# Performance work log

Hardware: AMD Instinct MI355X
Metric: run time of the kernel (lower is better)

Reference implementation:

```python
import jax, jax.numpy as jnp
import numpy as np

B, S, R, C_MSA, C_PAIR, H, D = 1, 128, 384, 256, 128, 8, 32
EPS = 1e-5


def setup_inputs() -> dict:
    key = jax.random.key(0)
    ks = jax.random.split(key, 8)
    w = 0.02
    return {
        "msa_repr": jax.random.normal(ks[0], (B, S, R, C_MSA), jnp.float32),
        "pair_repr": jax.random.normal(ks[1], (B, R, R, C_PAIR), jnp.float32),
        "ln_g": jnp.ones((R,), jnp.float32),
        "ln_b": jnp.zeros((R,), jnp.float32),
        "Wq": jax.random.normal(ks[2], (C_MSA, H * D), jnp.float32) * w,
        "Wk": jax.random.normal(ks[3], (C_MSA, H * D), jnp.float32) * w,
        "Wv": jax.random.normal(ks[4], (C_MSA, H * D), jnp.float32) * w,
        "Wb": jax.random.normal(ks[5], (C_PAIR, H), jnp.float32) * w,
        "bb": jnp.zeros((H,), jnp.float32),
        "Wg": jax.random.normal(ks[6], (C_MSA, H * D), jnp.float32) * w,
        "bg": jnp.zeros((H * D,), jnp.float32),
        "Wo": jax.random.normal(ks[7], (H * D, C_MSA), jnp.float32) * w,
        "bo": jnp.zeros((C_MSA,), jnp.float32),
    }


def reference(msa_repr, pair_repr, ln_g, ln_b, Wq, Wk, Wv, Wb, bb, Wg, bg, Wo, bo):
    b, s, r, c = msa_repr.shape
    scale = 1.0 / jnp.sqrt(jnp.float32(D))
    # LayerNorm over the residue axis r (module permutes b s r c -> b c s r and
    # normalizes the last dim = sequence_size), gamma/beta indexed by r.
    mu = jnp.mean(msa_repr, axis=2, keepdims=True)
    var = jnp.var(msa_repr, axis=2, keepdims=True)
    x = (msa_repr - mu) * jax.lax.rsqrt(var + EPS)
    x = x * ln_g[None, None, :, None] + ln_b[None, None, :, None]
    # flatten MSA rows into batch: (b*s, r, c)
    x = x.reshape(b * s, r, c)
    q = (x @ Wq).reshape(b * s, r, H, D).transpose(0, 2, 1, 3)  # (bs) h r d
    k = (x @ Wk).reshape(b * s, r, H, D).transpose(0, 2, 1, 3)
    v = (x @ Wv).reshape(b * s, r, H, D).transpose(0, 2, 1, 3)
    g = jax.nn.sigmoid(x @ Wg + bg).reshape(b * s, r, H, D).transpose(0, 2, 1, 3)
    # pair bias: b i j c -> b i j h -> b h i j, tiled over rows as in einops repeat '(a b)'
    bias = (pair_repr @ Wb + bb).transpose(0, 3, 1, 2)  # b h i j
    bias = jnp.tile(bias, (s, 1, 1, 1))  # (s*b) h i j (matches original (a b) order)
    dots = jnp.einsum('bhid,bhjd->bhij', q, k)  # (bs) h r r  -- dominant memory traffic
    attn = jax.nn.softmax(scale * dots + bias, axis=-1)
    out = jnp.einsum('bhij,bhjd->bhid', attn, v) * g  # (bs) h r d
    # '(b h) n w d -> b h w n d' with h=s, then concat heads along last dim
    out = out.reshape(b, s, H, r, D).transpose(0, 1, 3, 2, 4).reshape(b, s, r, H * D)
    return out @ Wo + bo  # b s r c
```

## Files before the change

kernel.cpp:

```cpp
#include <hip/hip_runtime.h>
#include <hip/hip_bf16.h>
#include <stdint.h>

typedef __attribute__((ext_vector_type(8))) short s16x8;
typedef __attribute__((ext_vector_type(4))) float f32x4;
typedef __attribute__((ext_vector_type(2))) float f32x2;

__device__ __forceinline__ ushort f2bf(float f){
  union { float f; uint32_t u; } v; v.f = f;
  uint32_t r = v.u + 0x7FFFu + ((v.u >> 16) & 1u);
  return (ushort)(r >> 16);
}
__device__ __forceinline__ float bf2f(ushort u){
  union { uint32_t u; float f; } v; v.u = ((uint32_t)u) << 16; return v.f;
}

__global__ __launch_bounds__(256) void ln_part(const float* __restrict__ msa,
    float* __restrict__ part){
  int s = blockIdx.x, rq = blockIdx.y, c = threadIdx.x;
  const float* p = msa + (size_t)s*98304 + (size_t)rq*48*256 + c;
  float sum = 0.f, sq = 0.f;
  for (int r = 0; r < 48; ++r){ float v = p[(size_t)r*256]; sum += v; sq += v*v; }
  f32x2* o = (f32x2*)part;
  o[((size_t)s*8 + rq)*256 + c] = (f32x2){sum, sq};
}

__global__ __launch_bounds__(256) void ln_stats(const float* __restrict__ part,
    float* __restrict__ stats){
  int s = blockIdx.x, c = threadIdx.x;
  const f32x2* p = (const f32x2*)part;
  float sum = 0.f, sq = 0.f;
  #pragma unroll
  for (int rq = 0; rq < 8; ++rq){
    f32x2 v = p[((size_t)s*8 + rq)*256 + c];
    sum += v.x; sq += v.y;
  }
  float mu = sum * (1.f/384.f);
  float var = sq * (1.f/384.f) - mu*mu;
  ((f32x2*)stats)[(size_t)s*256 + c] = (f32x2){mu, rsqrtf(var + 1e-5f)};
}

__global__ __launch_bounds__(256) void ln_apply(const float* __restrict__ msa,
    const float* __restrict__ stats, const float* __restrict__ ln_g,
    const float* __restrict__ ln_b, ushort* __restrict__ xbf){
  int s = blockIdx.x, rq = blockIdx.y, c = threadIdx.x;
  f32x2 st = ((const f32x2*)stats)[(size_t)s*256 + c];
  const float* p = msa + (size_t)s*98304 + (size_t)rq*48*256 + c;
  ushort* o = xbf + (size_t)s*98304 + (size_t)rq*48*256 + c;
  for (int r = 0; r < 48; ++r){
    int rr = rq*48 + r;
    float v = (p[(size_t)r*256] - st.x) * st.y * ln_g[rr] + ln_b[rr];
    o[(size_t)r*256] = f2bf(v);
  }
}

__global__ __launch_bounds__(256) void cvt_w(const float* __restrict__ Wq, const float* __restrict__ Wk,
    const float* __restrict__ Wv, const float* __restrict__ Wg, const float* __restrict__ Wo,
    ushort* __restrict__ out){
  int w = blockIdx.y;
  const float* W = (w==0)?Wq:(w==1)?Wk:(w==2)?Wv:(w==3)?Wg:Wo;
  int idx = blockIdx.x*256 + threadIdx.x;
  int k = idx >> 8, n = idx & 255;
  out[(size_t)w*65536 + (size_t)n*256 + k] = f2bf(W[idx]);
}

__global__ __launch_bounds__(256) void bias_kernel(const float* __restrict__ pair,
    const float* __restrict__ Wb, const float* __restrict__ bb, float* __restrict__ bias){
  __shared__ float pl[32*133];
  __shared__ float wb[128*8];
  int i = blockIdx.x, j0 = blockIdx.y*32, tid = threadIdx.x;
  for (int t = tid; t < 1024; t += 256) wb[t] = Wb[t];
  const float* src = pair + ((size_t)i*384 + j0)*128;
  for (int t = tid; t < 4096; t += 256){ int j = t>>7, c = t&127; pl[j*133 + c] = src[t]; }
  __syncthreads();
  int h = tid >> 5, jj = tid & 31;
  float acc = bb[h];
  const float* row = pl + jj*133;
  #pragma unroll 8
  for (int c = 0; c < 128; ++c) acc = fmaf(row[c], wb[c*8 + h], acc);
  bias[(size_t)h*147456 + (size_t)i*384 + (j0 + jj)] = acc;
}

__device__ __forceinline__ void gemm64x64(const ushort* __restrict__ A, const ushort* __restrict__ Bt,
                                          int m0, int lr, int lg, f32x4 acc[4][4]){
  #pragma unroll
  for (int ks = 0; ks < 8; ++ks){
    const int k0 = ks*32 + lg*8;
    s16x8 a[4], b[4];
    #pragma unroll
    for (int mt = 0; mt < 4; ++mt)
      a[mt] = *reinterpret_cast<const s16x8*>(A + (size_t)(m0 + mt*16 + lr)*256 + k0);
    #pragma unroll
    for (int nt = 0; nt < 4; ++nt)
      b[nt] = *reinterpret_cast<const s16x8*>(Bt + (size_t)(nt*16 + lr)*256 + k0);
    #pragma unroll
    for (int mt = 0; mt < 4; ++mt)
      #pragma unroll
      for (int nt = 0; nt < 4; ++nt)
        acc[mt][nt] = __builtin_amdgcn_mfma_f32_16x16x32_bf16(a[mt], b[nt], acc[mt][nt], 0, 0, 0);
  }
}

__global__ __launch_bounds__(512) void proj_kernel(const ushort* __restrict__ xbf,
    const ushort* __restrict__ wt_all, const float* __restrict__ bg,
    ushort* __restrict__ q, ushort* __restrict__ k, ushort* __restrict__ v, ushort* __restrict__ g){
  int w = blockIdx.y;
  const ushort* Bt = wt_all + (size_t)w*65536;
  int tid = threadIdx.x, wave = tid>>6, lane = tid&63, lr = lane&15, lg = lane>>4;
  int wm = wave>>2, wn = wave&3;
  int m0 = blockIdx.x*128 + wm*64;
  f32x4 acc[4][4];
  #pragma unroll
  for (int a=0;a<4;++a) for (int b=0;b<4;++b) acc[a][b] = (f32x4){0.f,0.f,0.f,0.f};
  gemm64x64(xbf, Bt + (size_t)(wn*64)*256, m0, lr, lg, acc);
  ushort* out = (w==0)?q:(w==1)?k:(w==2)?v:g;
  #pragma unroll
  for (int mt = 0; mt < 4; ++mt){
    int mrow = m0 + mt*16 + lg*4;
    int s = mrow/384, r = mrow - s*384;
    #pragma unroll
    for (int nt = 0; nt < 4; ++nt){
      int n = wn*64 + nt*16 + lr;
      int hh = n>>5, d = n&31;
      size_t o = (((size_t)s*8 + hh)*384 + r)*32 + d;
      #pragma unroll
      for (int t = 0; t < 4; ++t){
        float val = acc[mt][nt][t];
        if (w == 3) val = 1.0f/(1.0f + __expf(-(val + bg[n])));
        out[o + (size_t)t*32] = f2bf(val);
      }
    }
  }
}

#define VSTR 400
__global__ __launch_bounds__(512) void attn_kernel(const ushort* __restrict__ q,
    const ushort* __restrict__ kk, const ushort* __restrict__ vv, const ushort* __restrict__ gg,
    const float* __restrict__ bias, ushort* __restrict__ att_out){
  __shared__ ushort Kl[384*40];
  __shared__ ushort Vt[32*VSTR];
  const float SCALE = 0.17677669529663687f;
  int s = blockIdx.x, h = blockIdx.y, tid = threadIdx.x;
  const size_t base = ((size_t)s*8 + h)*384*32;
  for (int it = 0; it < 3; ++it){
    int idx = tid + it*512;
    int r = idx>>2, d0 = (idx&3)*8;
    int m = r>>5, a = (r>>3)&3, j = r&7;
    int rho = (2*m + (j>>2))*16 + 4*a + (j&3);
    s16x8 val = *reinterpret_cast<const s16x8*>(kk + base + (size_t)r*32 + d0);
    *reinterpret_cast<s16x8*>(&Kl[rho*40 + d0]) = val;
  }
  for (int it = 0; it < 3; ++it){
    int idx = tid + it*512;
    int r = idx>>2, d0 = (idx&3)*8;
    s16x8 val = *reinterpret_cast<const s16x8*>(vv + base + (size_t)r*32 + d0);
    #pragma unroll
    for (int j = 0; j < 8; ++j) Vt[(d0+j)*VSTR + r] = ((ushort*)&val)[j];
  }
  __syncthreads();
  int wave = tid>>6, lane = tid&63, lr = lane&15, lg = lane>>4;
  for (int itile = wave; itile < 24; itile += 8){
    int i0 = itile*16;
    s16x8 qf = *reinterpret_cast<const s16x8*>(q + base + (size_t)(i0 + lr)*32 + lg*8);
    const float* bp = bias + (size_t)h*147456 + (size_t)(i0 + lr)*384 + 8*lg;
    f32x4 acc0 = {0.f,0.f,0.f,0.f}, acc1 = {0.f,0.f,0.f,0.f};
    float rsum = 0.f;
    #pragma unroll 4
    for (int m = 0; m < 12; ++m){
      s16x8 kf0 = *reinterpret_cast<const s16x8*>(&Kl[((2*m+0)*16 + lr)*40 + lg*8]);
      s16x8 kf1 = *reinterpret_cast<const s16x8*>(&Kl[((2*m+1)*16 + lr)*40 + lg*8]);
      f32x4 d0 = __builtin_amdgcn_mfma_f32_16x16x32_bf16(kf0, qf, (f32x4){0.f,0.f,0.f,0.f}, 0, 0, 0);
      f32x4 d1 = __builtin_amdgcn_mfma_f32_16x16x32_bf16(kf1, qf, (f32x4){0.f,0.f,0.f,0.f}, 0, 0, 0);
      f32x4 bv0 = *reinterpret_cast<const f32x4*>(bp + 32*m);
      f32x4 bv1 = *reinterpret_cast<const f32x4*>(bp + 32*m + 4);
      s16x8 pa;
      #pragma unroll
      for (int t = 0; t < 4; ++t){
        float e0 = __expf(fmaf(d0[t], SCALE, bv0[t]));
        float e1 = __expf(fmaf(d1[t], SCALE, bv1[t]));
        rsum += e0 + e1;
        ((ushort*)&pa)[t]   = f2bf(e0);
        ((ushort*)&pa)[t+4] = f2bf(e1);
      }
      s16x8 vb0 = *reinterpret_cast<const s16x8*>(&Vt[lr*VSTR + 32*m + 8*lg]);
      s16x8 vb1 = *reinterpret_cast<const s16x8*>(&Vt[(16+lr)*VSTR + 32*m + 8*lg]);
      acc0 = __builtin_amdgcn_mfma_f32_16x16x32_bf16(pa, vb0, acc0, 0, 0, 0);
      acc1 = __builtin_amdgcn_mfma_f32_16x16x32_bf16(pa, vb1, acc1, 0, 0, 0);
    }
    rsum += __shfl_xor(rsum, 16);
    rsum += __shfl_xor(rsum, 32);
    const ushort* gp = gg + base + (size_t)(i0 + lg*4)*32;
    ushort* op = att_out + ((size_t)s*384 + i0 + lg*4)*256 + h*32;
    #pragma unroll
    for (int t = 0; t < 4; ++t){
      float inv = 1.0f / __shfl(rsum, 4*lg + t);
      float g0 = bf2f(gp[(size_t)t*32 + lr]);
      float g1 = bf2f(gp[(size_t)t*32 + 16 + lr]);
      op[(size_t)t*256 + lr]      = f2bf(acc0[t]*inv*g0);
      op[(size_t)t*256 + 16 + lr] = f2bf(acc1[t]*inv*g1);
    }
  }
}

__global__ __launch_bounds__(512) void oproj_kernel(const ushort* __restrict__ att,
    const ushort* __restrict__ Wot, const float* __restrict__ bo, float* __restrict__ out){
  int tid = threadIdx.x, wave = tid>>6, lane = tid&63, lr = lane&15, lg = lane>>4;
  int wm = wave>>2, wn = wave&3;
  int m0 = blockIdx.x*128 + wm*64;
  f32x4 acc[4][4];
  #pragma unroll
  for (int a=0;a<4;++a) for (int b=0;b<4;++b) acc[a][b] = (f32x4){0.f,0.f,0.f,0.f};
  gemm64x64(att, Wot + (size_t)(wn*64)*256, m0, lr, lg, acc);
  #pragma unroll
  for (int mt = 0; mt < 4; ++mt){
    int mrow = m0 + mt*16 + lg*4;
    #pragma unroll
    for (int nt = 0; nt < 4; ++nt){
      int n = wn*64 + nt*16 + lr;
      float bn = bo[n];
      #pragma unroll
      for (int t = 0; t < 4; ++t)
        out[(size_t)(mrow + t)*256 + n] = acc[mt][nt][t] + bn;
    }
  }
}

extern "C" void kernel_launch(void* const* d_in, const int* in_sizes, int n_in,
                              void* d_out, int out_size, void* d_ws, size_t ws_size,
                              hipStream_t stream){
  const float* msa  = (const float*)d_in[0];
  const float* pair = (const float*)d_in[1];
  const float* ln_g = (const float*)d_in[2];
  const float* ln_b = (const float*)d_in[3];
  const float* Wq   = (const float*)d_in[4];
  const float* Wk   = (const float*)d_in[5];
  const float* Wv   = (const float*)d_in[6];
  const float* Wb   = (const float*)d_in[7];
  const float* bb   = (const float*)d_in[8];
  const float* Wg   = (const float*)d_in[9];
  const float* bg   = (const float*)d_in[10];
  const float* Wo   = (const float*)d_in[11];
  const float* bo   = (const float*)d_in[12];
  float* out = (float*)d_out;
  char* ws = (char*)d_ws;
  const size_t SZ = (size_t)49152*256*2;
  ushort* xbf = (ushort*)(ws);
  ushort* qb  = (ushort*)(ws + SZ);
  ushort* kb  = (ushort*)(ws + 2*SZ);
  ushort* vb  = (ushort*)(ws + 3*SZ);
  ushort* gb  = (ushort*)(ws + 4*SZ);
  float*  bias= (float*)(ws + 5*SZ);
  ushort* wt  = (ushort*)(ws + 5*SZ + 4718592);
  ushort* att = xbf;
  float* part  = (float*)(ws + SZ);
  float* stats = (float*)(ws + SZ + 4*1024*1024);

  ln_part  <<<dim3(128,8),  dim3(256), 0, stream>>>(msa, part);
  ln_stats <<<dim3(128),    dim3(256), 0, stream>>>(part, stats);
  ln_apply <<<dim3(128,8),  dim3(256), 0, stream>>>(msa, stats, ln_g, ln_b, xbf);
  cvt_w      <<<dim3(256,5),   dim3(256), 0, stream>>>(Wq, Wk, Wv, Wg, Wo, wt);
  bias_kernel<<<dim3(384,12),  dim3(256), 0, stream>>>(pair, Wb, bb, bias);
  proj_kernel<<<dim3(384,4),   dim3(512), 0, stream>>>(xbf, wt, bg, qb, kb, vb, gb);
  attn_kernel<<<dim3(128,8),   dim3(512), 0, stream>>>(qb, kb, vb, gb, bias, att);
  oproj_kernel<<<dim3(384,1),  dim3(512), 0, stream>>>(att, wt + (size_t)4*65536, bo, out);
}
```

Before: 452.0 us.

## Stage GEMM A tiles into swizzled LDS via direct global-to-LDS loads

The projection and output-projection GEMMs now copy each 64-row A tile into shared memory using global_load_lds with an XOR swizzle, then read the MFMA fragments from LDS instead of straight from global memory. Blocks shrink from 512 threads covering 128 rows to 256 threads covering 64 rows, which doubles the grid, and launch bounds now request 4 blocks per CU. The aim is to share A across the four waves, cut redundant global/L2 reads and avoid bank conflicts. B is still read directly from global memory, and the new barrier means each block fully serialises its load phase against its compute phase.

```diff
diff --git a/kernel.cpp b/kernel.cpp
--- a/kernel.cpp
+++ b/kernel.cpp
@@ -5,6 +5,9 @@
 typedef __attribute__((ext_vector_type(8))) short s16x8;
 typedef __attribute__((ext_vector_type(4))) float f32x4;
 typedef __attribute__((ext_vector_type(2))) float f32x2;
+
+#define AS1(p) ((const __attribute__((address_space(1))) void*)(p))
+#define AS3(p) ((__attribute__((address_space(3))) void*)(p))
 
 __device__ __forceinline__ ushort f2bf(float f){
   union { float f; uint32_t u; } v; v.f = f;
@@ -81,18 +84,35 @@
   bias[(size_t)h*147456 + (size_t)i*384 + (j0 + jj)] = acc;
 }
 
-__device__ __forceinline__ void gemm64x64(const ushort* __restrict__ A, const ushort* __restrict__ Bt,
-                                          int m0, int lr, int lg, f32x4 acc[4][4]){
+__device__ __forceinline__ void stage_a64(const ushort* __restrict__ A, int m0,
+                                          ushort* Al, int tid){
+  int wave = tid>>6, lane = tid&63;
+  #pragma unroll
+  for (int it = 0; it < 8; ++it){
+    int chunk = wave*8 + it;
+    int base  = chunk*1024;
+    int beta  = base + lane*16;
+    int row   = beta>>9, cbs = beta&511;
+    int cb    = cbs ^ ((row&7)<<4);
+    const char* src = (const char*)A + (size_t)(m0+row)*512 + cb;
+    __builtin_amdgcn_global_load_lds(AS1(src), AS3((char*)Al + base), 16, 0, 0);
+  }
+}
+
+__device__ __forceinline__ void gemm64_lds(const ushort* Al, const ushort* __restrict__ Bt,
+                                           int lr, int lg, f32x4 acc[4][4]){
   #pragma unroll
   for (int ks = 0; ks < 8; ++ks){
-    const int k0 = ks*32 + lg*8;
     s16x8 a[4], b[4];
     #pragma unroll
-    for (int mt = 0; mt < 4; ++mt)
-      a[mt] = *reinterpret_cast<const s16x8*>(A + (size_t)(m0 + mt*16 + lr)*256 + k0);
+    for (int mt = 0; mt < 4; ++mt){
+      int row = mt*16 + lr;
+      int beta = row*512 + ((ks*64 + lg*16) ^ ((lr&7)<<4));
+      a[mt] = *reinterpret_cast<const s16x8*>((const char*)Al + beta);
+    }
     #pragma unroll
     for (int nt = 0; nt < 4; ++nt)
-      b[nt] = *reinterpret_cast<const s16x8*>(Bt + (size_t)(nt*16 + lr)*256 + k0);
+      b[nt] = *reinterpret_cast<const s16x8*>(Bt + (size_t)(nt*16 + lr)*256 + ks*32 + lg*8);
     #pragma unroll
     for (int mt = 0; mt < 4; ++mt)
       #pragma unroll
@@ -101,18 +121,20 @@
   }
 }
 
-__global__ __launch_bounds__(512) void proj_kernel(const ushort* __restrict__ xbf,
+__global__ __launch_bounds__(256, 4) void proj_kernel(const ushort* __restrict__ xbf,
     const ushort* __restrict__ wt_all, const float* __restrict__ bg,
     ushort* __restrict__ q, ushort* __restrict__ k, ushort* __restrict__ v, ushort* __restrict__ g){
+  __shared__ ushort Al[64*256];
   int w = blockIdx.y;
   const ushort* Bt = wt_all + (size_t)w*65536;
   int tid = threadIdx.x, wave = tid>>6, lane = tid&63, lr = lane&15, lg = lane>>4;
-  int wm = wave>>2, wn = wave&3;
-  int m0 = blockIdx.x*128 + wm*64;
+  int m0 = blockIdx.x*64;
+  stage_a64(xbf, m0, Al, tid);
+  __syncthreads();
   f32x4 acc[4][4];
   #pragma unroll
   for (int a=0;a<4;++a) for (int b=0;b<4;++b) acc[a][b] = (f32x4){0.f,0.f,0.f,0.f};
-  gemm64x64(xbf, Bt + (size_t)(wn*64)*256, m0, lr, lg, acc);
+  gemm64_lds(Al, Bt + (size_t)(wave*64)*256, lr, lg, acc);
   ushort* out = (w==0)?q:(w==1)?k:(w==2)?v:g;
   #pragma unroll
   for (int mt = 0; mt < 4; ++mt){
@@ -120,7 +142,7 @@
     int s = mrow/384, r = mrow - s*384;
     #pragma unroll
     for (int nt = 0; nt < 4; ++nt){
-      int n = wn*64 + nt*16 + lr;
+      int n = wave*64 + nt*16 + lr;
       int hh = n>>5, d = n&31;
       size_t o = (((size_t)s*8 + hh)*384 + r)*32 + d;
       #pragma unroll
@@ -202,21 +224,23 @@
   }
 }
 
-__global__ __launch_bounds__(512) void oproj_kernel(const ushort* __restrict__ att,
+__global__ __launch_bounds__(256, 4) void oproj_kernel(const ushort* __restrict__ att,
     const ushort* __restrict__ Wot, const float* __restrict__ bo, float* __restrict__ out){
+  __shared__ ushort Al[64*256];
   int tid = threadIdx.x, wave = tid>>6, lane = tid&63, lr = lane&15, lg = lane>>4;
-  int wm = wave>>2, wn = wave&3;
-  int m0 = blockIdx.x*128 + wm*64;
+  int m0 = blockIdx.x*64;
+  stage_a64(att, m0, Al, tid);
+  __syncthreads();
   f32x4 acc[4][4];
   #pragma unroll
   for (int a=0;a<4;++a) for (int b=0;b<4;++b) acc[a][b] = (f32x4){0.f,0.f,0.f,0.f};
-  gemm64x64(att, Wot + (size_t)(wn*64)*256, m0, lr, lg, acc);
+  gemm64_lds(Al, Wot + (size_t)(wave*64)*256, lr, lg, acc);
   #pragma unroll
   for (int mt = 0; mt < 4; ++mt){
     int mrow = m0 + mt*16 + lg*4;
     #pragma unroll
     for (int nt = 0; nt < 4; ++nt){
-      int n = wn*64 + nt*16 + lr;
+      int n = wave*64 + nt*16 + lr;
       float bn = bo[n];
       #pragma unroll
       for (int t = 0; t < 4; ++t)
@@ -260,7 +284,7 @@
   ln_apply <<<dim3(128,8),  dim3(256), 0, stream>>>(msa, stats, ln_g, ln_b, xbf);
   cvt_w      <<<dim3(256,5),   dim3(256), 0, stream>>>(Wq, Wk, Wv, Wg, Wo, wt);
   bias_kernel<<<dim3(384,12),  dim3(256), 0, stream>>>(pair, Wb, bb, bias);
-  proj_kernel<<<dim3(384,4),   dim3(512), 0, stream>>>(xbf, wt, bg, qb, kb, vb, gb);
+  proj_kernel<<<dim3(768,4),   dim3(256), 0, stream>>>(xbf, wt, bg, qb, kb, vb, gb);
   attn_kernel<<<dim3(128,8),   dim3(512), 0, stream>>>(qb, kb, vb, gb, bias, att);
-  oproj_kernel<<<dim3(384,1),  dim3(512), 0, stream>>>(att, wt + (size_t)4*65536, bo, out);
-}
+  oproj_kernel<<<dim3(768),    dim3(256), 0, stream>>>(att, wt + (size_t)4*65536, bo, out);
+}
```

Measured after the change: 389.3 us. -13.9%, faster.
